# Performance work log

Hardware: AMD Instinct MI355X
Metric: run time of the kernel (lower is better)

## Reference

```python
import jax, jax.numpy as jnp
import numpy as np

N_NODES = 100000
N_EDGES = 1600000
D_FEAT = 64
EPS_NORM = 1e-12  # torch F.normalize clamp


def setup_inputs() -> dict:
    key = jax.random.key(0)
    k1, k2, k3, k4 = jax.random.split(key, 4)
    x = jax.random.normal(k1, (N_NODES, D_FEAT), dtype=jnp.float32)
    row = jax.random.randint(k2, (N_EDGES,), 0, N_NODES, dtype=jnp.int32)
    offset = jax.random.randint(k3, (N_EDGES,), 1, N_NODES, dtype=jnp.int32)
    col = (row + offset) % N_NODES  # guarantees no self-loops
    edge_index = jnp.stack([row, col], axis=0)
    edge_attr = jax.random.uniform(k4, (N_EDGES,), dtype=jnp.float32)  # co-occurrence rates >= 0
    eps = jnp.zeros((1,), dtype=jnp.float32)
    beta = jnp.ones((1,), dtype=jnp.float32)
    return {"x": x, "edge_index": edge_index, "edge_attr": edge_attr, "eps": eps, "beta": beta}


def reference(x, edge_index, edge_attr, eps, beta):
    N, F = x.shape
    row, col = edge_index[0], edge_index[1]

    # Per-source-node L2 normalization of edge_attr (vectorized form of the
    # original python loop: edge_attr[row==i] = normalize(edge_attr[row==i], p=2))
    sq = jax.ops.segment_sum(edge_attr * edge_attr, row, num_segments=N)
    src_norm = jnp.maximum(jnp.sqrt(sq), EPS_NORM)
    ea = edge_attr / src_norm[row]

    # Add self loops with edge_attr = 1
    loop = jnp.arange(N, dtype=row.dtype)
    row2 = jnp.concatenate([row, loop])
    col2 = jnp.concatenate([col, loop])
    ea2 = jnp.concatenate([ea, jnp.ones((N,), dtype=ea.dtype)])

    # Row-wise L2 normalize node features
    xnorm = jnp.maximum(jnp.linalg.norm(x, axis=-1, keepdims=True), EPS_NORM)
    xn = x / xnorm

    # Segment softmax over edges grouped by source node (row)
    alpha = beta[0] * ea2
    amax = jax.ops.segment_max(alpha, row2, num_segments=N)
    e = jnp.exp(alpha - amax[row2])
    denom = jax.ops.segment_sum(e, row2, num_segments=N)
    alpha = e / denom[row2]

    # spmm: out[i] = sum_{(i,j) in E} alpha_ij * xn[j]
    out = jax.ops.segment_sum(alpha[:, None] * xn[col2], row2, num_segments=N)
    return (1.0 + eps[0]) * xn + out
```

## Files before the change

### kernel.cpp

```cpp
#include <hip/hip_runtime.h>
#include <math.h>

#define D 64
#define EPSN 1e-12f
#define RPB1 64
#define RPB1_SH 6
#define NBK_MAX 2048
#define CAPB 1280
#define CH 4096

__device__ __forceinline__ float bf2f(unsigned short u) {
    return __uint_as_float((unsigned)u << 16);
}
__device__ __forceinline__ unsigned short f2bf(float f) {
    unsigned u = __float_as_uint(f);
    u = (u + 0x7FFFu + ((u >> 16) & 1u)) >> 16;
    return (unsigned short)u;
}

__global__ __launch_bounds__(512) void k_xnp1(const int* __restrict__ row,
                                              const int* __restrict__ col,
                                              const float* __restrict__ ea,
                                              int* __restrict__ gcur1,
                                              float2* __restrict__ p1,
                                              const float4* __restrict__ x4,
                                              ushort4* __restrict__ xnh4,
                                              int E, int N, int p1b, int NBK1) {
    __shared__ unsigned hist[NBK_MAX];
    __shared__ unsigned gb[NBK_MAX];

    int tid = threadIdx.x;
    if ((int)blockIdx.x < p1b) {
        int base = blockIdx.x * CH;
        int end  = min(base + CH, E);

        for (int i = tid; i < NBK_MAX; i += 512) hist[i] = 0;
        __syncthreads();

        for (int j = base + tid; j < end; j += 512)
            atomicAdd(&hist[(unsigned)row[j] >> RPB1_SH], 1u);
        __syncthreads();

        for (int i = tid; i < NBK1; i += 512) {
            unsigned c = hist[i];
            if (c) gb[i] = (unsigned)(i * CAPB)
                         + (unsigned)atomicAdd(&gcur1[i], (int)c) - c;
        }
        __syncthreads();

        for (int j = base + tid; j < end; j += 512) {
            unsigned r = (unsigned)row[j];
            unsigned b = r >> RPB1_SH;
            unsigned gpos = gb[b] + atomicAdd(&hist[b], 1u);
            unsigned pk = ((r & (RPB1 - 1)) << 23) | (unsigned)col[j];
            p1[gpos] = make_float2(ea[j], __uint_as_float(pk));
        }
    } else {
        int t = (blockIdx.x - p1b) * 512 + tid;
        int r = t >> 4;
        int g = t & 15;
        if (r >= N) return;
        float4 v = x4[(size_t)r * 16 + g];
        float s = v.x * v.x + v.y * v.y + v.z * v.z + v.w * v.w;
        #pragma unroll
        for (int off = 8; off; off >>= 1) s += __shfl_xor(s, off);
        float inv = 1.0f / fmaxf(sqrtf(s), EPSN);
        ushort4 o;
        o.x = f2bf(v.x * inv); o.y = f2bf(v.y * inv);
        o.z = f2bf(v.z * inv); o.w = f2bf(v.w * inv);
        xnh4[(size_t)r * 16 + g] = o;
    }
}

template <int U>
__device__ __forceinline__ void gstep(const float2* __restrict__ lsrt, int k, unsigned lb,
                                      const char* __restrict__ xb,
                                      float& esum, float& acc) {
    float2 e[U];
    float xv[U];
    #pragma unroll
    for (int u = 0; u < U; ++u) e[u] = lsrt[k + u];
    #pragma unroll
    for (int u = 0; u < U; ++u)
        xv[u] = bf2f(*(const unsigned short*)(xb + (__float_as_uint(e[u].y) + lb)));
    #pragma unroll
    for (int u = 0; u < U; ++u) {
        esum += e[u].x;
        acc = fmaf(e[u].x, xv[u], acc);
    }
}

__global__ __launch_bounds__(512) void k_p2f(const int* __restrict__ gcnt,
                                             const float2* __restrict__ p1,
                                             const unsigned short* __restrict__ xnh,
                                             const float* __restrict__ beta,
                                             const float* __restrict__ eps,
                                             float* __restrict__ out, int N) {
    __shared__ float2   lsrt[CAPB];
    __shared__ unsigned lpack[RPB1];
    __shared__ unsigned ldeg[RPB1];
    __shared__ unsigned loff[RPB1];
    __shared__ unsigned lcur[RPB1];
    __shared__ float    lbinv[RPB1];

    int b = blockIdx.x;
    int rowbase = b << RPB1_SH;
    int nrows = min(RPB1, N - rowbase);
    if (nrows <= 0) return;
    int s = b * CAPB;
    int cnt = gcnt[b];
    int tid = threadIdx.x;
    int wv = tid >> 6, lane = tid & 63;
    const char* xb = (const char*)xnh;
    unsigned lb = (unsigned)lane << 1;

    if (tid < RPB1) lpack[tid] = 0;
    __syncthreads();

    for (int j = tid; j < cnt; j += 512) {
        float2 p = p1[s + j];
        unsigned rl = __float_as_uint(p.y) >> 23;
        unsigned q = __float2uint_rn(p.x * p.x * 32768.0f);
        atomicAdd(&lpack[rl], 0x400000u + q);
    }
    __syncthreads();

    unsigned dv = 0;
    if (tid < RPB1) {
        unsigned pk = lpack[tid];
        dv = pk >> 22;
        ldeg[tid] = dv;
        float sq = (float)(pk & 0x3FFFFFu) * (1.0f / 32768.0f);
        lbinv[tid] = beta[0] / fmaxf(sqrtf(sq), EPSN);
        loff[tid] = dv;
    }
    __syncthreads();
    for (int off = 1; off < RPB1; off <<= 1) {
        unsigned add = (tid < RPB1 && tid >= off) ? loff[tid - off] : 0;
        __syncthreads();
        if (tid < RPB1) loff[tid] += add;
        __syncthreads();
    }
    if (tid < RPB1) {
        unsigned ex = loff[tid] - dv;
        loff[tid] = ex;
        lcur[tid] = ex;
    }
    __syncthreads();

    for (int j = tid; j < cnt; j += 512) {
        float2 p = p1[s + j];
        unsigned pk = __float_as_uint(p.y);
        unsigned rl = pk >> 23;
        float w = __expf(p.x * lbinv[rl]);
        unsigned pos = atomicAdd(&lcur[rl], 1u);
        lsrt[pos] = make_float2(w, __uint_as_float((pk & 0x7FFFFFu) << 7));
    }
    __syncthreads();

    float ebv = __expf(beta[0]);
    float c1 = 1.0f + eps[0];
    for (int r = wv; r < nrows; r += 8) {
        int ks = (int)loff[r];
        int ke = ks + (int)ldeg[r];
        float esum = 0.0f, acc = 0.0f;
        int k = ks;
        for (; k + 16 <= ke; k += 16) gstep<16>(lsrt, k, lb, xb, esum, acc);
        if (k + 8 <= ke) { gstep<8>(lsrt, k, lb, xb, esum, acc); k += 8; }
        if (k + 4 <= ke) { gstep<4>(lsrt, k, lb, xb, esum, acc); k += 4; }
        for (; k < ke; ++k) {
            float2 e0 = lsrt[k];
            esum += e0.x;
            acc = fmaf(e0.x, bf2f(*(const unsigned short*)(xb + (__float_as_uint(e0.y) + lb))), acc);
        }
        int gr = rowbase + r;
        float xs = bf2f(*(const unsigned short*)(xb + (((unsigned)gr << 7) + lb)));
        float invden = 1.0f / (esum + ebv);
        out[((size_t)gr << 6) + lane] = c1 * xs + (acc + ebv * xs) * invden;
    }
}

static inline size_t align_up(size_t v, size_t a) { return (v + a - 1) & ~(a - 1); }

extern "C" void kernel_launch(void* const* d_in, const int* in_sizes, int n_in,
                              void* d_out, int out_size, void* d_ws, size_t ws_size,
                              hipStream_t stream) {
    const float* x    = (const float*)d_in[0];
    const int*   ei   = (const int*)d_in[1];
    const float* ea   = (const float*)d_in[2];
    const float* eps  = (const float*)d_in[3];
    const float* beta = (const float*)d_in[4];
    float* out = (float*)d_out;

    int N = in_sizes[0] / D;
    int E = in_sizes[2];
    const int* row = ei;
    const int* col = ei + E;
    int NBK1 = (N + RPB1 - 1) >> RPB1_SH;

    char* base = (char*)d_ws;
    size_t off = 0;
    unsigned short* xnh = (unsigned short*)(base + off); off = align_up(off + (size_t)N * D * sizeof(unsigned short), 256);
    int*    gcur1       = (int*)(base + off);            off = align_up(off + NBK_MAX * sizeof(int), 256);
    float2* p1buf       = (float2*)(base + off);

    hipMemsetAsync(gcur1, 0, NBK_MAX * sizeof(int), stream);

    int p1_blocks = (E + CH - 1) / CH;
    int xn_blocks = ((size_t)N * 16 + 511) / 512;

    k_xnp1<<<p1_blocks + xn_blocks, 512, 0, stream>>>(row, col, ea, gcur1, p1buf,
                                                      (const float4*)x, (ushort4*)xnh,
                                                      E, N, p1_blocks, NBK1);
    k_p2f <<<NBK1, 512, 0, stream>>>(gcur1, p1buf, xnh, beta, eps, out, N);
}
```

Baseline: 85.26 us.

## Bucket edges by 128-row groups and split each bucket across two blocks

The scatter pass now groups edges into buckets of 128 source rows instead of 64, which halves the number of buckets and so reduces per-chunk histogram work and global atomic contention. The gather kernel launches two blocks per bucket. Each block reads the whole bucket and keeps only the edges for its 64-row half, so every bucket is read twice from global memory. A cap check on the local sort buffer is added to guard against overflow on skewed buckets.

```diff
diff --git a/kernel.cpp b/kernel.cpp
--- a/kernel.cpp
+++ b/kernel.cpp
@@ -3,11 +3,13 @@
 
 #define D 64
 #define EPSN 1e-12f
-#define RPB1 64
-#define RPB1_SH 6
-#define NBK_MAX 2048
-#define CAPB 1280
+#define RPBC 128
+#define RPBC_SH 7
+#define NBK_MAX 1024
+#define CAPB 2560
 #define CH 4096
+#define SUBR 64
+#define CAPS 1344
 
 __device__ __forceinline__ float bf2f(unsigned short u) {
     return __uint_as_float((unsigned)u << 16);
@@ -38,7 +40,7 @@
         __syncthreads();
 
         for (int j = base + tid; j < end; j += 512)
-            atomicAdd(&hist[(unsigned)row[j] >> RPB1_SH], 1u);
+            atomicAdd(&hist[(unsigned)row[j] >> RPBC_SH], 1u);
         __syncthreads();
 
         for (int i = tid; i < NBK1; i += 512) {
@@ -50,9 +52,9 @@
 
         for (int j = base + tid; j < end; j += 512) {
             unsigned r = (unsigned)row[j];
-            unsigned b = r >> RPB1_SH;
+            unsigned b = r >> RPBC_SH;
             unsigned gpos = gb[b] + atomicAdd(&hist[b], 1u);
-            unsigned pk = ((r & (RPB1 - 1)) << 23) | (unsigned)col[j];
+            unsigned pk = ((r & (RPBC - 1)) << 23) | (unsigned)col[j];
             p1[gpos] = make_float2(ea[j], __uint_as_float(pk));
         }
     } else {
@@ -96,37 +98,42 @@
                                              const float* __restrict__ beta,
                                              const float* __restrict__ eps,
                                              float* __restrict__ out, int N) {
-    __shared__ float2   lsrt[CAPB];
-    __shared__ unsigned lpack[RPB1];
-    __shared__ unsigned ldeg[RPB1];
-    __shared__ unsigned loff[RPB1];
-    __shared__ unsigned lcur[RPB1];
-    __shared__ float    lbinv[RPB1];
-
-    int b = blockIdx.x;
-    int rowbase = b << RPB1_SH;
-    int nrows = min(RPB1, N - rowbase);
+    __shared__ float2   lsrt[CAPS];
+    __shared__ unsigned lpack[SUBR];
+    __shared__ unsigned ldeg[SUBR];
+    __shared__ unsigned loff[SUBR];
+    __shared__ unsigned lcur[SUBR];
+    __shared__ float    lbinv[SUBR];
+
+    int blk = blockIdx.x;
+    int cb   = blk >> 1;
+    int half = blk & 1;
+    int rlbase  = half << 6;
+    int rowbase = (cb << RPBC_SH) + rlbase;
+    int nrows = min(SUBR, N - rowbase);
     if (nrows <= 0) return;
-    int s = b * CAPB;
-    int cnt = gcnt[b];
+    int s = cb * CAPB;
+    int cnt = gcnt[cb];
     int tid = threadIdx.x;
     int wv = tid >> 6, lane = tid & 63;
     const char* xb = (const char*)xnh;
     unsigned lb = (unsigned)lane << 1;
 
-    if (tid < RPB1) lpack[tid] = 0;
+    if (tid < SUBR) lpack[tid] = 0;
     __syncthreads();
 
     for (int j = tid; j < cnt; j += 512) {
         float2 p = p1[s + j];
-        unsigned rl = __float_as_uint(p.y) >> 23;
-        unsigned q = __float2uint_rn(p.x * p.x * 32768.0f);
-        atomicAdd(&lpack[rl], 0x400000u + q);
+        int rl = (int)(__float_as_uint(p.y) >> 23) - rlbase;
+        if ((unsigned)rl < (unsigned)SUBR) {
+            unsigned q = __float2uint_rn(p.x * p.x * 32768.0f);
+            atomicAdd(&lpack[rl], 0x400000u + q);
+        }
     }
     __syncthreads();
 
     unsigned dv = 0;
-    if (tid < RPB1) {
+    if (tid < SUBR) {
         unsigned pk = lpack[tid];
         dv = pk >> 22;
         ldeg[tid] = dv;
@@ -135,13 +142,13 @@
         loff[tid] = dv;
     }
     __syncthreads();
-    for (int off = 1; off < RPB1; off <<= 1) {
-        unsigned add = (tid < RPB1 && tid >= off) ? loff[tid - off] : 0;
-        __syncthreads();
-        if (tid < RPB1) loff[tid] += add;
-        __syncthreads();
-    }
-    if (tid < RPB1) {
+    for (int off = 1; off < SUBR; off <<= 1) {
+        unsigned add = (tid < SUBR && tid >= off) ? loff[tid - off] : 0;
+        __syncthreads();
+        if (tid < SUBR) loff[tid] += add;
+        __syncthreads();
+    }
+    if (tid < SUBR) {
         unsigned ex = loff[tid] - dv;
         loff[tid] = ex;
         lcur[tid] = ex;
@@ -151,10 +158,12 @@
     for (int j = tid; j < cnt; j += 512) {
         float2 p = p1[s + j];
         unsigned pk = __float_as_uint(p.y);
-        unsigned rl = pk >> 23;
-        float w = __expf(p.x * lbinv[rl]);
-        unsigned pos = atomicAdd(&lcur[rl], 1u);
-        lsrt[pos] = make_float2(w, __uint_as_float((pk & 0x7FFFFFu) << 7));
+        int rl = (int)(pk >> 23) - rlbase;
+        if ((unsigned)rl < (unsigned)SUBR) {
+            float w = __expf(p.x * lbinv[rl]);
+            unsigned pos = atomicAdd(&lcur[rl], 1u);
+            if (pos < CAPS) lsrt[pos] = make_float2(w, __uint_as_float((pk & 0x7FFFFFu) << 7));
+        }
     }
     __syncthreads();
 
@@ -196,7 +205,7 @@
     int E = in_sizes[2];
     const int* row = ei;
     const int* col = ei + E;
-    int NBK1 = (N + RPB1 - 1) >> RPB1_SH;
+    int NBK1 = (N + RPBC - 1) >> RPBC_SH;
 
     char* base = (char*)d_ws;
     size_t off = 0;
@@ -212,5 +221,5 @@
     k_xnp1<<<p1_blocks + xn_blocks, 512, 0, stream>>>(row, col, ea, gcur1, p1buf,
                                                       (const float4*)x, (ushort4*)xnh,
                                                       E, N, p1_blocks, NBK1);
-    k_p2f <<<NBK1, 512, 0, stream>>>(gcur1, p1buf, xnh, beta, eps, out, N);
-}
+    k_p2f <<<NBK1 * 2, 512, 0, stream>>>(gcur1, p1buf, xnh, beta, eps, out, N);
+}
```

Result: slower. 88.00 us (+3.2%).
